# Kernel tuning notes

Measured on AMD Instinct MI355X. Metric: run time of the kernel, lower is better.

The kernel has to match this reference:

```python
import jax, jax.numpy as jnp
import numpy as np

NUM_MASKS = 255   # loop ids 0..254; id 255 is background
NUM_SEG = 256     # segment table size per batch element (ids 0..255)


def setup_inputs() -> dict:
    key = jax.random.key(0)
    k1, k2 = jax.random.split(key)
    b, c, h, w = 8, 256, 128, 128
    x = jax.random.normal(k1, (b, c, h, w), dtype=jnp.float32)
    mask = jax.random.randint(k2, (b, 1, h, w), 0, 256).astype(jnp.float32)
    return {"x": x, "mask": mask}


def reference(x, mask):
    b, c, h, w = x.shape
    hw = h * w
    # nearest interpolation to (h, w) is identity (mask already at that size)
    ids = mask.reshape(b, hw).astype(jnp.int32)          # (b, hw) segment ids 0..255
    x_sig = jax.nn.sigmoid(x.reshape(b, c, hw))          # (b, c, hw)

    # single-pass segment reduce: per-(batch, id) sums and pixel counts
    seg = (ids + jnp.arange(b, dtype=jnp.int32)[:, None] * NUM_SEG).reshape(-1)  # (b*hw,)
    counts = jax.ops.segment_sum(jnp.ones((b * hw,), x_sig.dtype), seg,
                                 num_segments=b * NUM_SEG).reshape(b, NUM_SEG)   # (b, 256)
    vals = x_sig.transpose(0, 2, 1).reshape(b * hw, c)                            # (b*hw, c)
    sums = jax.ops.segment_sum(vals, seg, num_segments=b * NUM_SEG)
    sums = sums.reshape(b, NUM_SEG, c)                                            # (b, 256, c)
    avg = sums / jnp.maximum(counts, 1.0)[:, :, None]                             # (b, 256, c)

    # gather per-pixel segment average; id 255 keeps label 0 (loop only covers 0..254)
    label = jnp.take_along_axis(avg, ids[:, :, None], axis=1)                     # (b, hw, c)
    is_bg = (ids == NUM_MASKS)[:, :, None]                                        # (b, hw, 1)
    label = jnp.where(is_bg, 0.0, label).transpose(0, 2, 1)                       # (b, c, hw)

    # ignore_bg=True: zero sigmoid activations on background pixels
    x_sig = jnp.where(is_bg.transpose(0, 2, 1), 0.0, x_sig)

    return jnp.mean((x_sig - label) ** 2)
```

## Files before the change

### kernel.cpp

```cpp
#include <hip/hip_runtime.h>

#define B 8
#define C 256
#define HW 16384
#define HALF 8192
#define NSEG 256
#define NCH 32
#define CHUNK 512
#define NROW (B * C)
#define NMAINBLK 512
#define ROWS_PER_BLK 4


typedef unsigned short ushort8 __attribute__((ext_vector_type(8)));

__device__ __forceinline__ float sigmoidf(float x) {
    float e = __expf(-x);
    return __builtin_amdgcn_rcpf(1.0f + e);
}

__device__ __forceinline__ void ldsAddF32(float* a, float v) {
    __attribute__((address_space(3))) float* p3 =
        (__attribute__((address_space(3))) float*)a;
    asm volatile("ds_add_f32 %0, %1" :: "v"(p3), "v"(v));
}

#define BAR_VMLG() asm volatile("s_waitcnt vmcnt(0) lgkmcnt(0)\ns_barrier" ::: "memory")
#define BAR_LG()   asm volatile("s_waitcnt lgkmcnt(0)\ns_barrier" ::: "memory")

__global__ __launch_bounds__(256) void hist_kernel(const float* __restrict__ mask,
                                                   int* __restrict__ hist,
                                                   unsigned char* __restrict__ ids8) {
    __shared__ int h[NSEG];
    const int blk = blockIdx.x;
    const int b = blk >> 5, ch = blk & 31;
    const int t = threadIdx.x;
    h[t] = 0;
    __syncthreads();

    const float2* m2 = (const float2*)(mask + (size_t)b * HW + ch * CHUNK);
    uchar2* o2 = (uchar2*)(ids8 + (size_t)b * HW + ch * CHUNK);
    float2 v = m2[t];
    int i0 = (int)v.x, i1 = (int)v.y;
    o2[t] = make_uchar2((unsigned char)i0, (unsigned char)i1);
    atomicAdd(&h[i0], 1);
    atomicAdd(&h[i1], 1);
    __syncthreads();
    hist[blk * NSEG + t] = h[t];
}

__global__ __launch_bounds__(256) void assign_kernel(const unsigned char* __restrict__ ids8,
                                                     const int* __restrict__ hist,
                                                     int* __restrict__ starts_h,
                                                     int* __restrict__ counts_g,
                                                     unsigned short* __restrict__ permt) {
    __shared__ int sc[NSEG];
    __shared__ int off[NSEG];
    const int blk = blockIdx.x;
    const int b = blk >> 5, ch = blk & 31;
    const int half = ch >> 4;
    const int t = threadIdx.x;

    int tot = 0, tot_h = 0, pre = 0;
    for (int c2 = 0; c2 < NCH; ++c2) {
        int v = hist[((b << 5) + c2) * NSEG + t];
        tot += v;
        if ((c2 >> 4) == half) {
            tot_h += v;
            if (c2 < ch) pre += v;
        }
    }
    sc[t] = tot_h;
    __syncthreads();
    for (int o = 1; o < NSEG; o <<= 1) {
        int v = (t >= o) ? sc[t - o] : 0;
        __syncthreads();
        sc[t] += v;
        __syncthreads();
    }
    int st = sc[t] - tot_h;
    off[t] = st + pre;
    if ((ch & 15) == 0) starts_h[(b * 2 + half) * NSEG + t] = st;
    if (ch == 0) counts_g[b * NSEG + t] = tot;
    __syncthreads();

    const unsigned char* idc = ids8 + (size_t)b * HW + ch * CHUNK;
    for (int j = 0; j < 2; ++j) {
        int pi = j * 256 + t;
        int id = idc[pi];
        int pos = atomicAdd(&off[id], 1);
        int p = (ch * CHUNK + pi) & (HALF - 1);
        int sidx = ((pos >> 11) << 11) | (((pos >> 3) & 3) << 9) | (((pos >> 5) & 63) << 3) | (pos & 7);
        permt[(size_t)(b * 2 + half) * HALF + sidx] = (unsigned short)p;
    }
}


#define STEP(ST, XV) {                                               \
    if (pos == nxt) {                                                \
        ldsAddF32(&bS[s], S); ldsAddF32(&bQ[s], Q);                  \
        S = 0.0f; Q = 0.0f;                                          \
        do { ++s; } while (ST[s + 1] <= pos);                        \
        nxt = ST[s + 1];                                             \
    }                                                                \
    float e = sigmoidf(XV);                                          \
    S += e; Q += e * e; ++pos;                                       \
}

#define GRP(BUF, ST, PP) {                                           \
    float xv0 = BUF[PP[0]], xv1 = BUF[PP[1]], xv2 = BUF[PP[2]],      \
          xv3 = BUF[PP[3]], xv4 = BUF[PP[4]], xv5 = BUF[PP[5]],      \
          xv6 = BUF[PP[6]], xv7 = BUF[PP[7]];                        \
    STEP(ST, xv0) STEP(ST, xv1) STEP(ST, xv2) STEP(ST, xv3)          \
    STEP(ST, xv4) STEP(ST, xv5) STEP(ST, xv6) STEP(ST, xv7)          \
}

#define GATHER(BUF, ST, P0, P1, P2, P3) {                            \
    int pos = t * 32;                                                \
    int lo = 0, hi = NSEG;                                           \
    while (hi - lo > 1) {                                            \
        int mid = (lo + hi) >> 1;                                    \
        if (ST[mid] <= pos) lo = mid; else hi = mid;                 \
    }                                                                \
    int s = lo;                                                      \
    int nxt = ST[s + 1];                                             \
    float S = 0.0f, Q = 0.0f;                                        \
    GRP(BUF, ST, P0) GRP(BUF, ST, P1) GRP(BUF, ST, P2) GRP(BUF, ST, P3) \
    ldsAddF32(&bS[s], S); ldsAddF32(&bQ[s], Q);                      \
}

#define STAGE8(SRC, DST) {                                           \
    _Pragma("unroll")                                                \
    for (int j = 0; j < 8; ++j) {                                    \
        int o = j * 1024 + t * 4;                                    \
        __builtin_amdgcn_global_load_lds(                            \
            (const __attribute__((address_space(1))) void*)((SRC) + o), \
            (__attribute__((address_space(3))) void*)((DST) + o), 16, 0, 0); \
    }                                                                \
}

__global__ __launch_bounds__(256) void main_kernel(const float* __restrict__ x,
                                                   const unsigned short* __restrict__ permt,
                                                   const int* __restrict__ starts_h,
                                                   const int* __restrict__ counts_g,
                                                   double* __restrict__ partials) {
    __shared__ float buf0[HALF];
    __shared__ float buf1[HALF];
    __shared__ int st0[NSEG + 1];
    __shared__ int st1[NSEG + 1];
    __shared__ float bS[NSEG];
    __shared__ float bQ[NSEG];
    __shared__ double wsum[4];

    const int blk = blockIdx.x;
    const int rbase = blk * ROWS_PER_BLK;
    const int b = rbase >> 8;
    const int t = threadIdx.x;
    const int w = t >> 6, l = t & 63;

    STAGE8(x + (size_t)rbase * HW, buf0);

    const ushort8* prA = (const ushort8*)(permt + (size_t)(b * 2 + 0) * HALF);
    const ushort8* prB = (const ushort8*)(permt + (size_t)(b * 2 + 1) * HALF);
    ushort8 pa0 = prA[(w << 8) + (0 << 6) + l];
    ushort8 pa1 = prA[(w << 8) + (1 << 6) + l];
    ushort8 pa2 = prA[(w << 8) + (2 << 6) + l];
    ushort8 pa3 = prA[(w << 8) + (3 << 6) + l];
    ushort8 pb0 = prB[(w << 8) + (0 << 6) + l];
    ushort8 pb1 = prB[(w << 8) + (1 << 6) + l];
    ushort8 pb2 = prB[(w << 8) + (2 << 6) + l];
    ushort8 pb3 = prB[(w << 8) + (3 << 6) + l];

    st0[t] = starts_h[(b * 2 + 0) * NSEG + t];
    st1[t] = starts_h[(b * 2 + 1) * NSEG + t];
    if (t == 0) { st0[NSEG] = HALF; st1[NSEG] = HALF; }
    bS[t] = 0.0f;
    bQ[t] = 0.0f;

    int n_t = counts_g[b * NSEG + t];
    double rn = (n_t > 0) ? 1.0 / (double)n_t : 0.0;
    double acc = 0.0;

    for (int r = 0; r < ROWS_PER_BLK; ++r) {
        const float* rowp = x + (size_t)(rbase + r) * HW;

        BAR_VMLG();
        STAGE8(rowp + HALF, buf1);
        GATHER(buf0, st0, pa0, pa1, pa2, pa3);

        BAR_VMLG();
        if (r + 1 < ROWS_PER_BLK) {
            STAGE8(rowp + HW, buf0);
        }
        GATHER(buf1, st1, pb0, pb1, pb2, pb3);

        BAR_LG();
        {
            float Sv = bS[t], Qv = bQ[t];
            if (t < NSEG - 1) acc += (double)Qv - (double)Sv * (double)Sv * rn;
            bS[t] = 0.0f;
            bQ[t] = 0.0f;
        }
    }

    double p = acc;
    #pragma unroll
    for (int o = 32; o > 0; o >>= 1) p += __shfl_down(p, o);
    if (l == 0) wsum[w] = p;
    __syncthreads();
    if (t == 0) partials[blk] = wsum[0] + wsum[1] + wsum[2] + wsum[3];
}

__global__ __launch_bounds__(256) void final_kernel(const double* __restrict__ partials,
                                                    float* __restrict__ out) {
    __shared__ double wsum[4];
    const int t = threadIdx.x;
    double p = partials[t] + partials[t + 256];
    #pragma unroll
    for (int o = 32; o > 0; o >>= 1) p += __shfl_down(p, o);
    const int lane = t & 63, w = t >> 6;
    if (lane == 0) wsum[w] = p;
    __syncthreads();
    if (t == 0) {
        double total = wsum[0] + wsum[1] + wsum[2] + wsum[3];
        out[0] = (float)(total / (double)((size_t)B * C * HW));
    }
}

extern "C" void kernel_launch(void* const* d_in, const int* in_sizes, int n_in,
                              void* d_out, int out_size, void* d_ws, size_t ws_size,
                              hipStream_t stream) {
    const float* x = (const float*)d_in[0];
    const float* mask = (const float*)d_in[1];
    float* out = (float*)d_out;

    char* ws = (char*)d_ws;
    int* hist = (int*)ws;
    unsigned char* ids8 = (unsigned char*)(ws + 262144);
    int* starts_h = (int*)(ws + 393216);
    int* counts_g = (int*)(ws + 409600);
    unsigned short* permt = (unsigned short*)(ws + 417792);
    double* partials = (double*)(ws + 679936);

    hist_kernel<<<B * NCH, 256, 0, stream>>>(mask, hist, ids8);
    assign_kernel<<<B * NCH, 256, 0, stream>>>(ids8, hist, starts_h, counts_g, permt);
    main_kernel<<<NMAINBLK, 256, 0, stream>>>(x, permt, starts_h, counts_g, partials);
    final_kernel<<<1, 256, 0, stream>>>(partials, out);
}
```

Measured before the change: 209.2 us.

## Pad segment runs to 32-element groups and drop per-step boundary checks

Each segment's sorted pixel run is padded to a multiple of 32 with sentinel indices, so every thread's 32 elements belong to one segment, looked up from a per-group segment table. This removes the binary search and the per-element boundary branch with its extra LDS atomics, leaving one atomic pair per thread. The main kernel moves to 512 threads per block to cover the padded length, which roughly doubles the gathered slots and adds sentinel masking. The hist kernel also pre-fills the padded permutation and table with sentinels.

Result: no change. 208.6 us (-0.3%).

```diff
diff --git a/kernel.cpp b/kernel.cpp
--- a/kernel.cpp
+++ b/kernel.cpp
@@ -4,6 +4,7 @@
 #define C 256
 #define HW 16384
 #define HALF 8192
+#define PADN 16384
 #define NSEG 256
 #define NCH 32
 #define CHUNK 512
@@ -30,7 +31,9 @@
 
 __global__ __launch_bounds__(256) void hist_kernel(const float* __restrict__ mask,
                                                    int* __restrict__ hist,
-                                                   unsigned char* __restrict__ ids8) {
+                                                   unsigned char* __restrict__ ids8,
+                                                   unsigned int* __restrict__ permp32,
+                                                   unsigned int* __restrict__ segtab32) {
     __shared__ int h[NSEG];
     const int blk = blockIdx.x;
     const int b = blk >> 5, ch = blk & 31;
@@ -45,15 +48,21 @@
     o2[t] = make_uchar2((unsigned char)i0, (unsigned char)i1);
     atomicAdd(&h[i0], 1);
     atomicAdd(&h[i1], 1);
+
+    unsigned int* pp = permp32 + (size_t)blk * 512;
+    pp[t] = 0xFFFFFFFFu;
+    pp[t + 256] = 0xFFFFFFFFu;
+    if (t < 8) segtab32[blk * 8 + t] = 0xFFFFFFFFu;
+
     __syncthreads();
     hist[blk * NSEG + t] = h[t];
 }
 
 __global__ __launch_bounds__(256) void assign_kernel(const unsigned char* __restrict__ ids8,
                                                      const int* __restrict__ hist,
-                                                     int* __restrict__ starts_h,
                                                      int* __restrict__ counts_g,
-                                                     unsigned short* __restrict__ permt) {
+                                                     unsigned char* __restrict__ segtab,
+                                                     unsigned short* __restrict__ permp) {
     __shared__ int sc[NSEG];
     __shared__ int off[NSEG];
     const int blk = blockIdx.x;
@@ -70,7 +79,8 @@
             if (c2 < ch) pre += v;
         }
     }
-    sc[t] = tot_h;
+    int pad32 = (tot_h + 31) & ~31;
+    sc[t] = pad32;
     __syncthreads();
     for (int o = 1; o < NSEG; o <<= 1) {
         int v = (t >= o) ? sc[t - o] : 0;
@@ -78,79 +88,64 @@
         sc[t] += v;
         __syncthreads();
     }
-    int st = sc[t] - tot_h;
-    off[t] = st + pre;
-    if ((ch & 15) == 0) starts_h[(b * 2 + half) * NSEG + t] = st;
+    int pstart = sc[t] - pad32;
+    off[t] = pstart + pre;
     if (ch == 0) counts_g[b * NSEG + t] = tot;
+    if ((ch & 15) == 0) {
+        for (int g = pstart >> 5; g < (pstart + pad32) >> 5; ++g)
+            segtab[(b * 2 + half) * 512 + g] = (unsigned char)t;
+    }
     __syncthreads();
 
     const unsigned char* idc = ids8 + (size_t)b * HW + ch * CHUNK;
+    unsigned short* pp = permp + (size_t)(b * 2 + half) * PADN;
     for (int j = 0; j < 2; ++j) {
         int pi = j * 256 + t;
         int id = idc[pi];
         int pos = atomicAdd(&off[id], 1);
         int p = (ch * CHUNK + pi) & (HALF - 1);
         int sidx = ((pos >> 11) << 11) | (((pos >> 3) & 3) << 9) | (((pos >> 5) & 63) << 3) | (pos & 7);
-        permt[(size_t)(b * 2 + half) * HALF + sidx] = (unsigned short)p;
-    }
-}
-
-
-#define STEP(ST, XV) {                                               \
-    if (pos == nxt) {                                                \
-        ldsAddF32(&bS[s], S); ldsAddF32(&bQ[s], Q);                  \
-        S = 0.0f; Q = 0.0f;                                          \
-        do { ++s; } while (ST[s + 1] <= pos);                        \
-        nxt = ST[s + 1];                                             \
+        pp[sidx] = (unsigned short)p;
+    }
+}
+
+
+#define PAD8(BUF, PP) {                                              \
+    _Pragma("unroll")                                                \
+    for (int k = 0; k < 8; ++k) {                                    \
+        int p = PP[k];                                               \
+        float e = sigmoidf(BUF[p & (HALF - 1)]);                     \
+        e = (p == 0xFFFF) ? 0.0f : e;                                \
+        S += e; Q += e * e;                                          \
     }                                                                \
-    float e = sigmoidf(XV);                                          \
-    S += e; Q += e * e; ++pos;                                       \
-}
-
-#define GRP(BUF, ST, PP) {                                           \
-    float xv0 = BUF[PP[0]], xv1 = BUF[PP[1]], xv2 = BUF[PP[2]],      \
-          xv3 = BUF[PP[3]], xv4 = BUF[PP[4]], xv5 = BUF[PP[5]],      \
-          xv6 = BUF[PP[6]], xv7 = BUF[PP[7]];                        \
-    STEP(ST, xv0) STEP(ST, xv1) STEP(ST, xv2) STEP(ST, xv3)          \
-    STEP(ST, xv4) STEP(ST, xv5) STEP(ST, xv6) STEP(ST, xv7)          \
-}
-
-#define GATHER(BUF, ST, P0, P1, P2, P3) {                            \
-    int pos = t * 32;                                                \
-    int lo = 0, hi = NSEG;                                           \
-    while (hi - lo > 1) {                                            \
-        int mid = (lo + hi) >> 1;                                    \
-        if (ST[mid] <= pos) lo = mid; else hi = mid;                 \
-    }                                                                \
-    int s = lo;                                                      \
-    int nxt = ST[s + 1];                                             \
+}
+
+#define GATHERP(BUF, SG, P0, P1, P2, P3) {                           \
     float S = 0.0f, Q = 0.0f;                                        \
-    GRP(BUF, ST, P0) GRP(BUF, ST, P1) GRP(BUF, ST, P2) GRP(BUF, ST, P3) \
-    ldsAddF32(&bS[s], S); ldsAddF32(&bQ[s], Q);                      \
-}
-
-#define STAGE8(SRC, DST) {                                           \
+    PAD8(BUF, P0) PAD8(BUF, P1) PAD8(BUF, P2) PAD8(BUF, P3)          \
+    ldsAddF32(&bS[SG], S); ldsAddF32(&bQ[SG], Q);                    \
+}
+
+#define STAGE4(SRC, DST) {                                           \
     _Pragma("unroll")                                                \
-    for (int j = 0; j < 8; ++j) {                                    \
-        int o = j * 1024 + t * 4;                                    \
+    for (int j = 0; j < 4; ++j) {                                    \
+        int o = j * 2048 + t * 4;                                    \
         __builtin_amdgcn_global_load_lds(                            \
             (const __attribute__((address_space(1))) void*)((SRC) + o), \
             (__attribute__((address_space(3))) void*)((DST) + o), 16, 0, 0); \
     }                                                                \
 }
 
-__global__ __launch_bounds__(256) void main_kernel(const float* __restrict__ x,
-                                                   const unsigned short* __restrict__ permt,
-                                                   const int* __restrict__ starts_h,
+__global__ __launch_bounds__(512) void main_kernel(const float* __restrict__ x,
+                                                   const unsigned short* __restrict__ permp,
+                                                   const unsigned char* __restrict__ segtab,
                                                    const int* __restrict__ counts_g,
                                                    double* __restrict__ partials) {
     __shared__ float buf0[HALF];
     __shared__ float buf1[HALF];
-    __shared__ int st0[NSEG + 1];
-    __shared__ int st1[NSEG + 1];
     __shared__ float bS[NSEG];
     __shared__ float bQ[NSEG];
-    __shared__ double wsum[4];
+    __shared__ double wsum[8];
 
     const int blk = blockIdx.x;
     const int rbase = blk * ROWS_PER_BLK;
@@ -158,10 +153,10 @@
     const int t = threadIdx.x;
     const int w = t >> 6, l = t & 63;
 
-    STAGE8(x + (size_t)rbase * HW, buf0);
-
-    const ushort8* prA = (const ushort8*)(permt + (size_t)(b * 2 + 0) * HALF);
-    const ushort8* prB = (const ushort8*)(permt + (size_t)(b * 2 + 1) * HALF);
+    STAGE4(x + (size_t)rbase * HW, buf0);
+
+    const ushort8* prA = (const ushort8*)(permp + (size_t)(b * 2 + 0) * PADN);
+    const ushort8* prB = (const ushort8*)(permp + (size_t)(b * 2 + 1) * PADN);
     ushort8 pa0 = prA[(w << 8) + (0 << 6) + l];
     ushort8 pa1 = prA[(w << 8) + (1 << 6) + l];
     ushort8 pa2 = prA[(w << 8) + (2 << 6) + l];
@@ -171,13 +166,11 @@
     ushort8 pb2 = prB[(w << 8) + (2 << 6) + l];
     ushort8 pb3 = prB[(w << 8) + (3 << 6) + l];
 
-    st0[t] = starts_h[(b * 2 + 0) * NSEG + t];
-    st1[t] = starts_h[(b * 2 + 1) * NSEG + t];
-    if (t == 0) { st0[NSEG] = HALF; st1[NSEG] = HALF; }
-    bS[t] = 0.0f;
-    bQ[t] = 0.0f;
-
-    int n_t = counts_g[b * NSEG + t];
+    const int sgA = segtab[(b * 2 + 0) * 512 + t];
+    const int sgB = segtab[(b * 2 + 1) * 512 + t];
+
+    if (t < NSEG) { bS[t] = 0.0f; bQ[t] = 0.0f; }
+    int n_t = (t < NSEG) ? counts_g[b * NSEG + t] : 0;
     double rn = (n_t > 0) ? 1.0 / (double)n_t : 0.0;
     double acc = 0.0;
 
@@ -185,17 +178,17 @@
         const float* rowp = x + (size_t)(rbase + r) * HW;
 
         BAR_VMLG();
-        STAGE8(rowp + HALF, buf1);
-        GATHER(buf0, st0, pa0, pa1, pa2, pa3);
+        STAGE4(rowp + HALF, buf1);
+        GATHERP(buf0, sgA, pa0, pa1, pa2, pa3);
 
         BAR_VMLG();
         if (r + 1 < ROWS_PER_BLK) {
-            STAGE8(rowp + HW, buf0);
+            STAGE4(rowp + HW, buf0);
         }
-        GATHER(buf1, st1, pb0, pb1, pb2, pb3);
+        GATHERP(buf1, sgB, pb0, pb1, pb2, pb3);
 
         BAR_LG();
-        {
+        if (t < NSEG) {
             float Sv = bS[t], Qv = bQ[t];
             if (t < NSEG - 1) acc += (double)Qv - (double)Sv * (double)Sv * rn;
             bS[t] = 0.0f;
@@ -208,7 +201,12 @@
     for (int o = 32; o > 0; o >>= 1) p += __shfl_down(p, o);
     if (l == 0) wsum[w] = p;
     __syncthreads();
-    if (t == 0) partials[blk] = wsum[0] + wsum[1] + wsum[2] + wsum[3];
+    if (t == 0) {
+        double tt = 0.0;
+        #pragma unroll
+        for (int i = 0; i < 8; ++i) tt += wsum[i];
+        partials[blk] = tt;
+    }
 }
 
 __global__ __launch_bounds__(256) void final_kernel(const double* __restrict__ partials,
@@ -237,13 +235,14 @@
     char* ws = (char*)d_ws;
     int* hist = (int*)ws;
     unsigned char* ids8 = (unsigned char*)(ws + 262144);
-    int* starts_h = (int*)(ws + 393216);
-    int* counts_g = (int*)(ws + 409600);
-    unsigned short* permt = (unsigned short*)(ws + 417792);
-    double* partials = (double*)(ws + 679936);
-
-    hist_kernel<<<B * NCH, 256, 0, stream>>>(mask, hist, ids8);
-    assign_kernel<<<B * NCH, 256, 0, stream>>>(ids8, hist, starts_h, counts_g, permt);
-    main_kernel<<<NMAINBLK, 256, 0, stream>>>(x, permt, starts_h, counts_g, partials);
+    int* counts_g = (int*)(ws + 393216);
+    unsigned char* segtab = (unsigned char*)(ws + 401408);
+    unsigned short* permp = (unsigned short*)(ws + 409600);
+    double* partials = (double*)(ws + 933888);
+
+    hist_kernel<<<B * NCH, 256, 0, stream>>>(mask, hist, ids8,
+                                             (unsigned int*)permp, (unsigned int*)segtab);
+    assign_kernel<<<B * NCH, 256, 0, stream>>>(ids8, hist, counts_g, segtab, permp);
+    main_kernel<<<NMAINBLK, 512, 0, stream>>>(x, permp, segtab, counts_g, partials);
     final_kernel<<<1, 256, 0, stream>>>(partials, out);
 }
```
